# Kernel tuning notes

Measured on AMD Instinct MI355X. Metric: run time of the kernel, lower is better.

Reference implementation:

```python
import jax, jax.numpy as jnp
import numpy as np

TEMPERATURE = 1.0  # SpriteAssembler.compositing_temperature
EPS = 1e-6


def setup_inputs() -> dict:
    key = jax.random.key(0)
    k1, k2 = jax.random.split(key)
    B, H, W, N = 8, 256, 256, 64
    shapes = jax.random.uniform(k1, (B, H, W, N), dtype=jnp.float32)  # occupancy in [0,1]
    depths = jax.random.normal(k2, (B, N), dtype=jnp.float32)
    return {"shapes": shapes, "depths": depths}


def reference(shapes, depths):
    # custom_composite: depth-ordered log-space alpha compositing.
    # mask_i = s_i * prod_j (1 - s_j) ** tanh(relu((d_j - d_i)/T)), then normalize.
    d = depths / max(TEMPERATURE, 1e-6)                      # [B, N]
    s = jnp.clip(shapes, EPS, 1.0 - EPS)                     # [B, H, W, N]
    # occlusion weights: w[b, i, j] = tanh(relu(d_j - d_i))
    w = jnp.tanh(jax.nn.relu(d[:, None, :] - d[:, :, None]))  # [B, N, N]
    log1m = jnp.log1p(-s)                                    # log(1 - s), [B, H, W, N]
    # log_mask_i = log(s_i) + sum_j log(1 - s_j) * w[i, j]  (j == i term is 0 since w[i,i]=0)
    log_masks = jnp.log(s) + jnp.einsum('bhwj,bij->bhwi', log1m, w)
    unnormalized = jnp.exp(log_masks)                        # [B, H, W, N]
    masks = unnormalized / (jnp.sum(unnormalized, axis=-1, keepdims=True) + EPS)
    return masks
```

## Files before the change

kernel.cpp:

```cpp
#include <hip/hip_runtime.h>


typedef __attribute__((ext_vector_type(8))) _Float16 half8;
typedef __attribute__((ext_vector_type(4))) float floatx4;

#define EPSF 1e-6f

__device__ inline float fast_exp2(float x){ return __builtin_amdgcn_exp2f(x); }
__device__ inline float fast_log2(float x){ return __builtin_amdgcn_logf(x); }
__device__ inline float fast_rcp (float x){ return __builtin_amdgcn_rcpf(x); }

__global__ __launch_bounds__(256, 2) void sprite_mfma_kernel(
    const float* __restrict__ shapes,
    const float* __restrict__ depths,
    float* __restrict__ out)
{
    const int wave  = threadIdx.x >> 6;
    const int lane  = threadIdx.x & 63;
    const int batch = blockIdx.x >> 7;
    const int rblk  = blockIdx.x & 127;
    const int wid   = rblk * 4 + wave;

    __shared__ float dsh[64];
    if (threadIdx.x < 64) dsh[threadIdx.x] = depths[batch * 64 + threadIdx.x];
    __syncthreads();

    const int c = lane & 15;
    const int q = lane >> 4;

    half8 Bf[4][4];
    #pragma unroll
    for (int nt = 0; nt < 4; ++nt) {
        float di = dsh[nt * 16 + c];
        #pragma unroll
        for (int kt = 0; kt < 2; ++kt) {
            half8 h;
            #pragma unroll
            for (int jj = 0; jj < 8; ++jj) {
                int j = kt * 32 + q * 8 + jj;
                float x = fmaxf(dsh[j] - di, 0.0f);
                float e = fast_exp2(x * 2.885390082f);
                h[jj] = (_Float16)((e - 1.0f) * fast_rcp(e + 1.0f));
            }
            Bf[nt][kt] = h;
        }
        #pragma unroll
        for (int kt = 2; kt < 4; ++kt) {
            half8 h;
            #pragma unroll
            for (int jj = 0; jj < 8; ++jj) {
                int j = (kt - 2) * 32 + q * 8 + jj;
                h[jj] = (j == nt * 16 + c) ? (_Float16)1.0f : (_Float16)0.0f;
            }
            Bf[nt][kt] = h;
        }
    }

    const long pxbase = (long)batch * 65536 + (long)wid * 128;
    const float* sp = shapes + (pxbase + c) * 64 + q * 8;
    float* op = out + pxbase * 64;

    float4 pf0 = *(const float4*)(sp);
    float4 pf1 = *(const float4*)(sp + 4);
    float4 pf2 = *(const float4*)(sp + 32);
    float4 pf3 = *(const float4*)(sp + 36);

    for (int tile = 0; tile < 8; ++tile) {
        float4 s0 = pf0, s1 = pf1, s2 = pf2, s3 = pf3;
        if (tile < 7) {
            const float* sn = sp + (tile + 1) * 16 * 64;
            pf0 = *(const float4*)(sn);
            pf1 = *(const float4*)(sn + 4);
            pf2 = *(const float4*)(sn + 32);
            pf3 = *(const float4*)(sn + 36);
        }

        float sv[16] = {s0.x, s0.y, s0.z, s0.w, s1.x, s1.y, s1.z, s1.w,
                        s2.x, s2.y, s2.z, s2.w, s3.x, s3.y, s3.z, s3.w};
        half8 A_L_lo, A_L_hi, A_S_lo, A_S_hi;
        #pragma unroll
        for (int e = 0; e < 8; ++e) {
            float slo = fminf(fmaxf(sv[e],     EPSF), 1.0f - EPSF);
            float shi = fminf(fmaxf(sv[8 + e], EPSF), 1.0f - EPSF);
            A_L_lo[e] = (_Float16)fast_log2(1.0f - slo);
            A_S_lo[e] = (_Float16)fast_log2(slo);
            A_L_hi[e] = (_Float16)fast_log2(1.0f - shi);
            A_S_hi[e] = (_Float16)fast_log2(shi);
        }

        floatx4 acc[4];
        #pragma unroll
        for (int nt = 0; nt < 4; ++nt) {
            floatx4 a = {0.f, 0.f, 0.f, 0.f};
            a = __builtin_amdgcn_mfma_f32_16x16x32_f16(A_L_lo, Bf[nt][0], a, 0, 0, 0);
            a = __builtin_amdgcn_mfma_f32_16x16x32_f16(A_L_hi, Bf[nt][1], a, 0, 0, 0);
            a = __builtin_amdgcn_mfma_f32_16x16x32_f16(A_S_lo, Bf[nt][2], a, 0, 0, 0);
            a = __builtin_amdgcn_mfma_f32_16x16x32_f16(A_S_hi, Bf[nt][3], a, 0, 0, 0);
            acc[nt] = a;
        }

        float u[4][4];
        #pragma unroll
        for (int nt = 0; nt < 4; ++nt) {
            #pragma unroll
            for (int r = 0; r < 4; ++r) u[nt][r] = fast_exp2(acc[nt][r]);
        }

        #pragma unroll
        for (int r = 0; r < 4; ++r) {
            float tot = (u[0][r] + u[1][r]) + (u[2][r] + u[3][r]);
            tot += __shfl_xor(tot, 1, 64);
            tot += __shfl_xor(tot, 2, 64);
            tot += __shfl_xor(tot, 4, 64);
            tot += __shfl_xor(tot, 8, 64);
            float inv = fast_rcp(tot + EPSF);
            float* orow = op + (long)(tile * 16 + q * 4 + r) * 64 + c;
            orow[0]  = u[0][r] * inv;
            orow[16] = u[1][r] * inv;
            orow[32] = u[2][r] * inv;
            orow[48] = u[3][r] * inv;
        }
    }
}

extern "C" void kernel_launch(void* const* d_in, const int* in_sizes, int n_in,
                              void* d_out, int out_size, void* d_ws, size_t ws_size,
                              hipStream_t stream) {
    const float* shapes = (const float*)d_in[0];
    const float* depths = (const float*)d_in[1];
    float* out = (float*)d_out;
    sprite_mfma_kernel<<<1024, 256, 0, stream>>>(shapes, depths, out);
}
```

Before: 236.9 us.

## Transpose MFMA operands, apply log(s) term multiplicatively, vectorize output stores

The occlusion weight matrix becomes the A operand and the log(1-s) values become B, so the accumulator layout gives each lane four consecutive sprite values for one pixel. The log(s) term is no longer folded into the MFMA through an identity block. Instead s is reloaded in the output layout and multiplied after exp2, which halves the MFMA count and removes two log2s per element. Output writes become float4 stores and the row sum needs only two shuffles. Each block now covers half as many pixels, so the grid doubles. The kernel reads shapes twice, relying on cache hits for the second read.

```diff
diff --git a/kernel.cpp b/kernel.cpp
--- a/kernel.cpp
+++ b/kernel.cpp
@@ -17,8 +17,8 @@
 {
     const int wave  = threadIdx.x >> 6;
     const int lane  = threadIdx.x & 63;
-    const int batch = blockIdx.x >> 7;
-    const int rblk  = blockIdx.x & 127;
+    const int batch = blockIdx.x >> 8;
+    const int rblk  = blockIdx.x & 255;
     const int wid   = rblk * 4 + wave;
 
     __shared__ float dsh[64];
@@ -28,10 +28,10 @@
     const int c = lane & 15;
     const int q = lane >> 4;
 
-    half8 Bf[4][4];
+    half8 Aw[4][2];
     #pragma unroll
-    for (int nt = 0; nt < 4; ++nt) {
-        float di = dsh[nt * 16 + c];
+    for (int it = 0; it < 4; ++it) {
+        float di = dsh[it * 16 + c];
         #pragma unroll
         for (int kt = 0; kt < 2; ++kt) {
             half8 h;
@@ -42,83 +42,78 @@
                 float e = fast_exp2(x * 2.885390082f);
                 h[jj] = (_Float16)((e - 1.0f) * fast_rcp(e + 1.0f));
             }
-            Bf[nt][kt] = h;
-        }
-        #pragma unroll
-        for (int kt = 2; kt < 4; ++kt) {
-            half8 h;
-            #pragma unroll
-            for (int jj = 0; jj < 8; ++jj) {
-                int j = (kt - 2) * 32 + q * 8 + jj;
-                h[jj] = (j == nt * 16 + c) ? (_Float16)1.0f : (_Float16)0.0f;
-            }
-            Bf[nt][kt] = h;
+            Aw[it][kt] = h;
         }
     }
 
-    const long pxbase = (long)batch * 65536 + (long)wid * 128;
-    const float* sp = shapes + (pxbase + c) * 64 + q * 8;
-    float* op = out + pxbase * 64;
+    const long pxbase = (long)batch * 65536 + (long)wid * 64;
+    const float* sp = shapes + (pxbase + c) * 64;
+    float* op = out + (pxbase + c) * 64;
 
-    float4 pf0 = *(const float4*)(sp);
-    float4 pf1 = *(const float4*)(sp + 4);
-    float4 pf2 = *(const float4*)(sp + 32);
-    float4 pf3 = *(const float4*)(sp + 36);
+    float4 pf0 = *(const float4*)(sp + q * 8);
+    float4 pf1 = *(const float4*)(sp + q * 8 + 4);
+    float4 pf2 = *(const float4*)(sp + q * 8 + 32);
+    float4 pf3 = *(const float4*)(sp + q * 8 + 36);
 
-    for (int tile = 0; tile < 8; ++tile) {
+    for (int tile = 0; tile < 4; ++tile) {
+        const float* srow = sp + tile * 16 * 64;
+
         float4 s0 = pf0, s1 = pf1, s2 = pf2, s3 = pf3;
-        if (tile < 7) {
-            const float* sn = sp + (tile + 1) * 16 * 64;
+        if (tile < 3) {
+            const float* sn = srow + 16 * 64 + q * 8;
             pf0 = *(const float4*)(sn);
             pf1 = *(const float4*)(sn + 4);
             pf2 = *(const float4*)(sn + 32);
             pf3 = *(const float4*)(sn + 36);
         }
 
+        float4 sg[4];
+        #pragma unroll
+        for (int it = 0; it < 4; ++it)
+            sg[it] = *(const float4*)(srow + it * 16 + q * 4);
+
         float sv[16] = {s0.x, s0.y, s0.z, s0.w, s1.x, s1.y, s1.z, s1.w,
                         s2.x, s2.y, s2.z, s2.w, s3.x, s3.y, s3.z, s3.w};
-        half8 A_L_lo, A_L_hi, A_S_lo, A_S_hi;
+        half8 B_lo, B_hi;
         #pragma unroll
         for (int e = 0; e < 8; ++e) {
             float slo = fminf(fmaxf(sv[e],     EPSF), 1.0f - EPSF);
             float shi = fminf(fmaxf(sv[8 + e], EPSF), 1.0f - EPSF);
-            A_L_lo[e] = (_Float16)fast_log2(1.0f - slo);
-            A_S_lo[e] = (_Float16)fast_log2(slo);
-            A_L_hi[e] = (_Float16)fast_log2(1.0f - shi);
-            A_S_hi[e] = (_Float16)fast_log2(shi);
+            B_lo[e] = (_Float16)fast_log2(1.0f - slo);
+            B_hi[e] = (_Float16)fast_log2(1.0f - shi);
         }
 
         floatx4 acc[4];
         #pragma unroll
-        for (int nt = 0; nt < 4; ++nt) {
+        for (int it = 0; it < 4; ++it) {
             floatx4 a = {0.f, 0.f, 0.f, 0.f};
-            a = __builtin_amdgcn_mfma_f32_16x16x32_f16(A_L_lo, Bf[nt][0], a, 0, 0, 0);
-            a = __builtin_amdgcn_mfma_f32_16x16x32_f16(A_L_hi, Bf[nt][1], a, 0, 0, 0);
-            a = __builtin_amdgcn_mfma_f32_16x16x32_f16(A_S_lo, Bf[nt][2], a, 0, 0, 0);
-            a = __builtin_amdgcn_mfma_f32_16x16x32_f16(A_S_hi, Bf[nt][3], a, 0, 0, 0);
-            acc[nt] = a;
+            a = __builtin_amdgcn_mfma_f32_16x16x32_f16(Aw[it][0], B_lo, a, 0, 0, 0);
+            a = __builtin_amdgcn_mfma_f32_16x16x32_f16(Aw[it][1], B_hi, a, 0, 0, 0);
+            acc[it] = a;
         }
 
         float u[4][4];
+        float tot = 0.f;
         #pragma unroll
-        for (int nt = 0; nt < 4; ++nt) {
+        for (int it = 0; it < 4; ++it) {
             #pragma unroll
-            for (int r = 0; r < 4; ++r) u[nt][r] = fast_exp2(acc[nt][r]);
+            for (int r = 0; r < 4; ++r) {
+                float s = fminf(fmaxf(sg[it][r], EPSF), 1.0f - EPSF);
+                float v = fast_exp2(acc[it][r]) * s;
+                u[it][r] = v;
+                tot += v;
+            }
         }
+        tot += __shfl_xor(tot, 16, 64);
+        tot += __shfl_xor(tot, 32, 64);
+        float inv = fast_rcp(tot + EPSF);
 
+        float* orow = op + tile * 16 * 64;
         #pragma unroll
-        for (int r = 0; r < 4; ++r) {
-            float tot = (u[0][r] + u[1][r]) + (u[2][r] + u[3][r]);
-            tot += __shfl_xor(tot, 1, 64);
-            tot += __shfl_xor(tot, 2, 64);
-            tot += __shfl_xor(tot, 4, 64);
-            tot += __shfl_xor(tot, 8, 64);
-            float inv = fast_rcp(tot + EPSF);
-            float* orow = op + (long)(tile * 16 + q * 4 + r) * 64 + c;
-            orow[0]  = u[0][r] * inv;
-            orow[16] = u[1][r] * inv;
-            orow[32] = u[2][r] * inv;
-            orow[48] = u[3][r] * inv;
+        for (int it = 0; it < 4; ++it) {
+            float4 o = {u[it][0] * inv, u[it][1] * inv,
+                        u[it][2] * inv, u[it][3] * inv};
+            *(float4*)(orow + it * 16 + q * 4) = o;
         }
     }
 }
@@ -129,5 +124,5 @@
     const float* shapes = (const float*)d_in[0];
     const float* depths = (const float*)d_in[1];
     float* out = (float*)d_out;
-    sprite_mfma_kernel<<<1024, 256, 0, stream>>>(shapes, depths, out);
+    sprite_mfma_kernel<<<2048, 256, 0, stream>>>(shapes, depths, out);
 }
```

Measured after the change: 253.8 us. +7.1%, slower.
